# Kernel optimization log

Hardware: AMD Instinct MI355X
Metric: run time of the kernel (lower is better)

The kernel has to match this reference:

```python
import jax, jax.numpy as jnp
import numpy as np

DELTA = 0.0          # init kwarg (torch default is 0.7; 0.0 used so random data selects pairs)
N, T = 1_048_576, 32  # samples x trait columns
COS_EPS = 1e-8       # torch.cosine_similarity eps


def setup_inputs() -> dict:
    key = jax.random.key(0)
    k1, k2 = jax.random.split(key)
    return {
        "y_pred": jax.random.normal(k1, (N, T), dtype=jnp.float32),
        "y_true": jax.random.normal(k2, (N, T), dtype=jnp.float32),
    }


def reference(y_pred, y_true):
    t = y_true.shape[1]
    # Pearson correlation matrix over columns of y_true (centered Gram + norm outer)
    xc = y_true - jnp.mean(y_true, axis=0, keepdims=True)      # [N, T]
    nx = jnp.sqrt(jnp.sum(xc * xc, axis=0))                    # [T]
    pcc = jnp.einsum('nj,nk->jk', xc, xc) / (nx[:, None] * nx[None, :])
    # Cosine similarity matrix over columns of y_pred
    pn = jnp.sqrt(jnp.sum(y_pred * y_pred, axis=0))            # [T]
    denom = jnp.maximum(pn[:, None] * pn[None, :], COS_EPS)
    cos = jnp.einsum('nj,nk->jk', y_pred, y_pred) / denom      # [T, T]
    # Pair mask: 1 <= j < k < T (loop starts at j=1 in the original)
    idx = jnp.arange(t)
    pair_mask = (idx[None, :] > idx[:, None]) & (idx[:, None] >= 1)
    sel = pair_mask & (pcc >= DELTA)
    c = (t - 1) * (t - 2) // 2                                 # total pair count (incl. unselected)
    total = jnp.sum(jnp.where(sel, 1.0 - cos, 0.0))
    return total / c
```

## Files before the change

kernel.cpp:

```cpp
#include <hip/hip_runtime.h>

#define N_ROWS   1048576
#define T_COLS   32
#define NBLK     512
#define BLOCK    1024
#define WAVES    16
#define ROWS_PER_WAVE 256
#define CH       16
#define NWS      2080
#define NREP     64

typedef _Float16 half8    __attribute__((ext_vector_type(8)));
typedef float    floatx16 __attribute__((ext_vector_type(16)));

#define CHUNK_BYTES 2048
#define WAVE_BYTES  (2 * CHUNK_BYTES)
#define LDS_BYTES   (WAVES * WAVE_BYTES)

__global__ __launch_bounds__(BLOCK, 8) void ts_gram(const float* __restrict__ y_pred,
                                                    const float* __restrict__ y_true,
                                                    float* __restrict__ ws) {
    __shared__ alignas(16) char smem[LDS_BYTES];

    const int tid  = threadIdx.x;
    const int wv   = tid >> 6;
    const int mtx  = wv >> 3;
    const int sub  = wv & 7;
    const int lane = tid & 63;
    const int hi   = lane >> 5;
    const int col  = lane & 31;

    const float* src = (mtx == 0) ? y_true : y_pred;
    const size_t row0 = (size_t)blockIdx.x * (8 * ROWS_PER_WAVE) + (size_t)sub * ROWS_PER_WAVE;
    const float* gp = src + (row0 + (size_t)(lane >> 3)) * T_COLS + (lane & 7) * 4;

    char* lbase = smem + wv * WAVE_BYTES;

#define ISSUE(c) do {                                                         \
        char* lb_ = lbase + (((c) & 1) * CHUNK_BYTES);                        \
        const float* g_ = gp + (size_t)((c) * 16) * T_COLS;                   \
        __builtin_amdgcn_global_load_lds(                                     \
            (const __attribute__((address_space(1))) void*)g_,                \
            (__attribute__((address_space(3))) void*)lb_, 16, 0, 0);          \
        __builtin_amdgcn_global_load_lds(                                     \
            (const __attribute__((address_space(1))) void*)(g_ + 8 * T_COLS), \
            (__attribute__((address_space(3))) void*)(lb_ + 1024), 16, 0, 0); \
    } while (0)

    floatx16 acc = {};
    float cs = 0.0f;

    ISSUE(0);
    ISSUE(1);

    #pragma unroll
    for (int c = 0; c < CH; ++c) {
        if (c + 1 < CH) { asm volatile("s_waitcnt vmcnt(2)" ::: "memory"); }
        else            { asm volatile("s_waitcnt vmcnt(0)" ::: "memory"); }
        __builtin_amdgcn_sched_barrier(0);

        const float* rp = (const float*)(lbase + (c & 1) * CHUNK_BYTES)
                          + (size_t)hi * 8 * T_COLS + col;
        float v[8];
        #pragma unroll
        for (int j = 0; j < 8; ++j) v[j] = rp[j * T_COLS];

        asm volatile("s_waitcnt lgkmcnt(0)" ::: "memory");
        __builtin_amdgcn_sched_barrier(0);
        if (c + 2 < CH) ISSUE(c + 2);

        half8 h;
        #pragma unroll
        for (int j = 0; j < 8; ++j) h[j] = (_Float16)v[j];
        if (mtx == 0) {
            #pragma unroll
            for (int j = 0; j < 8; ++j) cs += v[j];
        }
        acc = __builtin_amdgcn_mfma_f32_32x32x16_f16(h, h, acc, 0, 0, 0);
    }
#undef ISSUE

    __syncthreads();
    float* s_red = (float*)smem;
    for (int i = tid; i < NWS; i += BLOCK) s_red[i] = 0.0f;
    __syncthreads();
    #pragma unroll
    for (int r = 0; r < 16; ++r) {
        int row = (r & 3) + 8 * (r >> 2) + 4 * hi;
        atomicAdd(&s_red[mtx * 1024 + row * 32 + col], acc[r]);
    }
    if (mtx == 0) {
        cs += __shfl_xor(cs, 32);
        if (lane < 32) atomicAdd(&s_red[2048 + col], cs);
    }
    __syncthreads();
    float* wsr = ws + (size_t)(blockIdx.x & (NREP - 1)) * NWS;
    for (int i = tid; i < NWS; i += BLOCK) atomicAdd(&wsr[i], s_red[i]);
}

__global__ __launch_bounds__(1024) void ts_final(const float* __restrict__ w,
                                                 float* __restrict__ out) {
    __shared__ float s_w[NWS];
    __shared__ float s_S[32], s_nx[32], s_pn[32];
    __shared__ float s_red[16];
    const int tid = threadIdx.x;
    const float invN = 1.0f / (float)N_ROWS;

    for (int i = tid; i < NWS; i += 1024) {
        float t = 0.0f;
        #pragma unroll 4
        for (int r = 0; r < NREP; ++r) t += w[(size_t)r * NWS + i];
        s_w[i] = t;
    }
    __syncthreads();

    if (tid < 32) {
        float S = s_w[2048 + tid];
        s_S[tid] = S;
        float d = s_w[tid * 32 + tid] - S * S * invN;
        s_nx[tid] = sqrtf(d);
        s_pn[tid] = sqrtf(s_w[1024 + tid * 33]);
    }
    __syncthreads();

    const int j = tid >> 5, k = tid & 31;
    float contrib = 0.0f;
    if (j >= 1 && k > j && j < 32) {
        float gc  = s_w[j * 32 + k] - s_S[j] * s_S[k] * invN;
        float pcc = gc / (s_nx[j] * s_nx[k]);
        float cs  = s_w[1024 + j * 32 + k] / fmaxf(s_pn[j] * s_pn[k], 1e-8f);
        if (pcc >= 0.0f) contrib = 1.0f - cs;
    }
    #pragma unroll
    for (int off = 32; off > 0; off >>= 1) contrib += __shfl_down(contrib, off);
    if ((tid & 63) == 0) s_red[tid >> 6] = contrib;
    __syncthreads();
    if (tid == 0) {
        float tot = 0.0f;
        #pragma unroll
        for (int i = 0; i < 16; ++i) tot += s_red[i];
        out[0] = tot * (1.0f / 465.0f);
    }
}

extern "C" void kernel_launch(void* const* d_in, const int* in_sizes, int n_in,
                              void* d_out, int out_size, void* d_ws, size_t ws_size,
                              hipStream_t stream) {
    const float* y_pred = (const float*)d_in[0];
    const float* y_true = (const float*)d_in[1];
    float* out = (float*)d_out;
    float* ws  = (float*)d_ws;

    hipMemsetAsync(ws, 0, (size_t)NREP * NWS * sizeof(float), stream);
    ts_gram<<<NBLK, BLOCK, 0, stream>>>(y_pred, y_true, ws);
    ts_final<<<1, 1024, 0, stream>>>(ws, out);
}
```

Before: 324.5 us.

## Replace async global-to-LDS loads with a deep register prefetch pipeline

Replaces the double-buffered global_load_lds pipeline with a 6-deep register prefetch of nontemporal vector loads, which are then staged into LDS for the transposed MFMA read. Blocks shrink to 512 threads with 8 waves, and each wave now processes 512 rows in 32 chunks. The column-sum for the mean moves to the staging step and is reduced via lane shuffles. The aim is more memory-level parallelism per wave to hide latency on a bandwidth-bound stream. The cost is more registers, and the LDS handoff no longer has explicit waits or barriers, so it relies on intra-wave ordering.

```diff
diff --git a/kernel.cpp b/kernel.cpp
--- a/kernel.cpp
+++ b/kernel.cpp
@@ -3,82 +3,85 @@
 #define N_ROWS   1048576
 #define T_COLS   32
 #define NBLK     512
-#define BLOCK    1024
-#define WAVES    16
-#define ROWS_PER_WAVE 256
-#define CH       16
+#define BLOCK    512
+#define WAVES_PB 8
+#define ROWS_PER_WAVE 512
+#define CH       32
+#define DEPTH    6
 #define NWS      2080
 #define NREP     64
 
 typedef _Float16 half8    __attribute__((ext_vector_type(8)));
+typedef float    f32x4    __attribute__((ext_vector_type(4)));
 typedef float    floatx16 __attribute__((ext_vector_type(16)));
 
-#define CHUNK_BYTES 2048
-#define WAVE_BYTES  (2 * CHUNK_BYTES)
-#define LDS_BYTES   (WAVES * WAVE_BYTES)
+#define CHUNK_FLOATS 512
+#define WAVE_BYTES   (2 * CHUNK_FLOATS * 4)
+#define LDS_BYTES    (WAVES_PB * WAVE_BYTES)
 
-__global__ __launch_bounds__(BLOCK, 8) void ts_gram(const float* __restrict__ y_pred,
+__global__ __launch_bounds__(BLOCK, 4) void ts_gram(const float* __restrict__ y_pred,
                                                     const float* __restrict__ y_true,
                                                     float* __restrict__ ws) {
     __shared__ alignas(16) char smem[LDS_BYTES];
 
     const int tid  = threadIdx.x;
     const int wv   = tid >> 6;
-    const int mtx  = wv >> 3;
-    const int sub  = wv & 7;
+    const int mtx  = wv >> 2;
+    const int sub  = wv & 3;
     const int lane = tid & 63;
     const int hi   = lane >> 5;
     const int col  = lane & 31;
+    const int lr   = lane >> 3;
+    const int lg   = lane & 7;
 
     const float* src = (mtx == 0) ? y_true : y_pred;
-    const size_t row0 = (size_t)blockIdx.x * (8 * ROWS_PER_WAVE) + (size_t)sub * ROWS_PER_WAVE;
-    const float* gp = src + (row0 + (size_t)(lane >> 3)) * T_COLS + (lane & 7) * 4;
+    const size_t row0 = (size_t)blockIdx.x * (4 * ROWS_PER_WAVE) + (size_t)sub * ROWS_PER_WAVE;
+    const f32x4* gp = (const f32x4*)(src + (row0 + (size_t)lr) * T_COLS) + lg;
 
-    char* lbase = smem + wv * WAVE_BYTES;
+    float* lds = (float*)(smem + wv * WAVE_BYTES);
 
-#define ISSUE(c) do {                                                         \
-        char* lb_ = lbase + (((c) & 1) * CHUNK_BYTES);                        \
-        const float* g_ = gp + (size_t)((c) * 16) * T_COLS;                   \
-        __builtin_amdgcn_global_load_lds(                                     \
-            (const __attribute__((address_space(1))) void*)g_,                \
-            (__attribute__((address_space(3))) void*)lb_, 16, 0, 0);          \
-        __builtin_amdgcn_global_load_lds(                                     \
-            (const __attribute__((address_space(1))) void*)(g_ + 8 * T_COLS), \
-            (__attribute__((address_space(3))) void*)(lb_ + 1024), 16, 0, 0); \
+    f32x4 pf[DEPTH][2];
+    floatx16 acc = {};
+    float cs[4] = {0.f, 0.f, 0.f, 0.f};
+
+#define LOADC(c, s) do {                                                     \
+        pf[s][0] = __builtin_nontemporal_load(&gp[((c) * 16 + 0) * 8]);      \
+        pf[s][1] = __builtin_nontemporal_load(&gp[((c) * 16 + 8) * 8]);      \
     } while (0)
 
-    floatx16 acc = {};
-    float cs = 0.0f;
+#define STAGEC(c, s) do {                                                    \
+        float* wp_ = lds + ((c) & 1) * CHUNK_FLOATS + lr * T_COLS + lg * 4;  \
+        _Pragma("unroll")                                                    \
+        for (int q_ = 0; q_ < 2; ++q_) {                                     \
+            *(f32x4*)(wp_ + q_ * 8 * T_COLS) = pf[s][q_];                    \
+            if (mtx == 0) {                                                  \
+                cs[0] += pf[s][q_][0]; cs[1] += pf[s][q_][1];                \
+                cs[2] += pf[s][q_][2]; cs[3] += pf[s][q_][3];                \
+            }                                                                \
+        }                                                                    \
+    } while (0)
 
-    ISSUE(0);
-    ISSUE(1);
+    #pragma unroll
+    for (int c = 0; c < DEPTH; ++c) LOADC(c, c);
+    STAGEC(0, 0);
 
     #pragma unroll
     for (int c = 0; c < CH; ++c) {
-        if (c + 1 < CH) { asm volatile("s_waitcnt vmcnt(2)" ::: "memory"); }
-        else            { asm volatile("s_waitcnt vmcnt(0)" ::: "memory"); }
-        __builtin_amdgcn_sched_barrier(0);
+        if (c + 1 < CH) STAGEC(c + 1, (c + 1) % DEPTH);
+        if (c + DEPTH < CH) LOADC(c + DEPTH, c % DEPTH);
 
-        const float* rp = (const float*)(lbase + (c & 1) * CHUNK_BYTES)
-                          + (size_t)hi * 8 * T_COLS + col;
+        const float* rp = lds + (c & 1) * CHUNK_FLOATS + hi * 8 * T_COLS + col;
         float v[8];
         #pragma unroll
         for (int j = 0; j < 8; ++j) v[j] = rp[j * T_COLS];
 
-        asm volatile("s_waitcnt lgkmcnt(0)" ::: "memory");
-        __builtin_amdgcn_sched_barrier(0);
-        if (c + 2 < CH) ISSUE(c + 2);
-
         half8 h;
         #pragma unroll
         for (int j = 0; j < 8; ++j) h[j] = (_Float16)v[j];
-        if (mtx == 0) {
-            #pragma unroll
-            for (int j = 0; j < 8; ++j) cs += v[j];
-        }
         acc = __builtin_amdgcn_mfma_f32_32x32x16_f16(h, h, acc, 0, 0, 0);
     }
-#undef ISSUE
+#undef LOADC
+#undef STAGEC
 
     __syncthreads();
     float* s_red = (float*)smem;
@@ -90,8 +93,16 @@
         atomicAdd(&s_red[mtx * 1024 + row * 32 + col], acc[r]);
     }
     if (mtx == 0) {
-        cs += __shfl_xor(cs, 32);
-        if (lane < 32) atomicAdd(&s_red[2048 + col], cs);
+        #pragma unroll
+        for (int k = 0; k < 4; ++k) {
+            cs[k] += __shfl_xor(cs[k], 8);
+            cs[k] += __shfl_xor(cs[k], 16);
+            cs[k] += __shfl_xor(cs[k], 32);
+        }
+        if (lr == 0) {
+            #pragma unroll
+            for (int k = 0; k < 4; ++k) atomicAdd(&s_red[2048 + lg * 4 + k], cs[k]);
+        }
     }
     __syncthreads();
     float* wsr = ws + (size_t)(blockIdx.x & (NREP - 1)) * NWS;
```

Result: slower. 338.6 us (+4.3%).
